# Kernel optimization log

Hardware: AMD Instinct MI355X
Metric: run time of the kernel (lower is better)

## Reference

```python
import jax, jax.numpy as jnp
import numpy as np

B, T, R = 128, 20, 49           # batch, caption length, num regions (7x7)
V, E, H, FD, A = 10000, 512, 512, 512, 256  # vocab, embed, hidden, feature, attn dims


def setup_inputs() -> dict:
    key = jax.random.key(0)
    ks = jax.random.split(key, 16)
    s = 0.02
    return {
        "features": jax.random.normal(ks[0], (B, R, FD), dtype=jnp.float32),
        "captions": jax.random.randint(ks[1], (B, T), 0, V),
        "emb": jax.random.normal(ks[2], (V, E), dtype=jnp.float32) * s,
        "W_h": jax.random.normal(ks[3], (A, H), dtype=jnp.float32) * s,
        "b_h": jnp.zeros((A,), jnp.float32),
        "W_f": jax.random.normal(ks[4], (A, FD), dtype=jnp.float32) * s,
        "b_f": jnp.zeros((A,), jnp.float32),
        "v_w": jax.random.normal(ks[5], (A,), dtype=jnp.float32) * s,
        "v_b": jnp.zeros((), jnp.float32),
        "W_ih": jax.random.normal(ks[6], (4 * H, E + FD), dtype=jnp.float32) * s,
        "W_hh": jax.random.normal(ks[7], (4 * H, H), dtype=jnp.float32) * s,
        "b_ih": jnp.zeros((4 * H,), jnp.float32),
        "b_hh": jnp.zeros((4 * H,), jnp.float32),
        "fc_W": jax.random.normal(ks[8], (V, H), dtype=jnp.float32) * s,
        "fc_b": jnp.zeros((V,), jnp.float32),
    }


def reference(features, captions, emb, W_h, b_h, W_f, b_f, v_w, v_b,
              W_ih, W_hh, b_ih, b_hh, fc_W, fc_b):
    Bn = features.shape[0]
    Hd = W_hh.shape[1]
    # features are constant across timesteps -> project once (same math as per-step W_f(features))
    f_proj = jnp.einsum('brf,af->bra', features, W_f) + b_f  # (B,R,A)
    embeds = emb[captions[:, :-1]]                            # (B,T-1,E)
    xs = jnp.swapaxes(embeds, 0, 1)                           # (T-1,B,E)
    bias = b_ih + b_hh

    def step(carry, x_t):
        hx, cx = carry
        # Bahdanau attention
        h = hx @ W_h.T + b_h                                  # (B,A)
        scores = jnp.tanh(h[:, None, :] + f_proj) @ v_w + v_b  # (B,R)
        alpha = jax.nn.softmax(scores, axis=1)
        context = jnp.einsum('br,brf->bf', alpha, features)   # (B,FD)
        # LSTMCell (PyTorch gate order: i,f,g,o)
        lstm_in = jnp.concatenate([x_t, context], axis=1)     # (B,E+FD)
        gates = lstm_in @ W_ih.T + hx @ W_hh.T + bias         # (B,4H)
        i, f, g, o = jnp.split(gates, 4, axis=1)
        cx = jax.nn.sigmoid(f) * cx + jax.nn.sigmoid(i) * jnp.tanh(g)
        hx = jax.nn.sigmoid(o) * jnp.tanh(cx)
        logit = hx @ fc_W.T + fc_b                            # (B,V)
        return (hx, cx), logit

    init = (jnp.zeros((Bn, Hd), features.dtype), jnp.zeros((Bn, Hd), features.dtype))
    _, logits = jax.lax.scan(step, init, xs)                  # (T-1,B,V)
    return jnp.swapaxes(logits, 0, 1)                         # (B,T-1,V)
```

## Files before the change

### kernel.cpp

```cpp
#include <hip/hip_runtime.h>
#include <hip/hip_bf16.h>
#include <math.h>

#define NB 128
#define NT 20
#define NS 19
#define NR 49
#define NV 10000
#define NE 512
#define NH 512
#define NFD 512
#define NA 256
#define NG 2048
#define NK2 1024

typedef __bf16 bf16_t;
typedef bf16_t bf16x8 __attribute__((ext_vector_type(8)));
typedef bf16_t bf16x4 __attribute__((ext_vector_type(4)));
typedef float f32x4 __attribute__((ext_vector_type(4)));

__device__ __forceinline__ float sigm(float x) { return 1.f / (1.f + expf(-x)); }

__device__ __forceinline__ void cvt8(bf16_t* d, const float* s) {
    float4 a = *(const float4*)s;
    float4 b = *(const float4*)(s + 4);
    bf16x8 v;
    v[0] = (bf16_t)a.x; v[1] = (bf16_t)a.y; v[2] = (bf16_t)a.z; v[3] = (bf16_t)a.w;
    v[4] = (bf16_t)b.x; v[5] = (bf16_t)b.y; v[6] = (bf16_t)b.z; v[7] = (bf16_t)b.w;
    *(bf16x8*)d = v;
}

__global__ __launch_bounds__(256) void k_prep(
    const float* __restrict__ fc_W, const float* __restrict__ W_ih,
    const float* __restrict__ W_hh, const float* __restrict__ W_h,
    const float* __restrict__ W_f, const float* __restrict__ features,
    const float* __restrict__ emb, const int* __restrict__ captions,
    const float* __restrict__ b_ih, const float* __restrict__ b_hh,
    const float* __restrict__ b_f, const float* __restrict__ b_h,
    bf16_t* __restrict__ fcWb, bf16_t* __restrict__ Wcat2,
    bf16_t* __restrict__ Wxg, bf16_t* __restrict__ W_hb,
    bf16_t* __restrict__ Wfb, bf16_t* __restrict__ featb,
    bf16_t* __restrict__ linx, float* __restrict__ bias,
    float* __restrict__ bfh, float* __restrict__ hx, float* __restrict__ cx,
    unsigned* __restrict__ flags)
{
    int g = blockIdx.x * 256 + threadIdx.x;
    if (g < 640000) { int idx = g * 8; cvt8(fcWb + idx, fc_W + idx); return; }
    g -= 640000;
    if (g < 262144) {
        int idx = g * 8;
        int row = idx >> 10, col = idx & 1023;
        int orig = (row & 3) * NH + (row >> 2);
        const float* src = (col < 512) ? (W_ih + (size_t)orig * 1024 + 512 + col)
                                       : (W_hh + (size_t)orig * 512 + (col - 512));
        cvt8(Wcat2 + idx, src);
        return;
    }
    g -= 262144;
    if (g < 131072) {
        int idx = g * 8;
        int row = idx >> 9, col = idx & 511;
        int orig = (row & 3) * NH + (row >> 2);
        cvt8(Wxg + idx, W_ih + (size_t)orig * 1024 + col);
        return;
    }
    g -= 131072;
    if (g < 16384) { int idx = g * 8; cvt8(W_hb + idx, W_h + idx); return; }
    g -= 16384;
    if (g < 16384) { int idx = g * 8; cvt8(Wfb + idx, W_f + idx); return; }
    g -= 16384;
    if (g < 401408) { int idx = g * 8; cvt8(featb + idx, features + idx); return; }
    g -= 401408;
    if (g < 155648) {
        int idx = g * 8;
        int row = idx >> 9, col = idx & 511;
        int t = row >> 7, b = row & 127;
        int cap = captions[b * NT + t];
        cvt8(linx + idx, emb + (size_t)cap * NE + col);
        return;
    }
    g -= 155648;
    if (g < 256) {
        int n0 = g * 8;
        #pragma unroll
        for (int i = 0; i < 8; ++i) {
            int n = n0 + i, h = n >> 2, gg = n & 3;
            int orig = gg * NH + h;
            bias[n] = b_ih[orig] + b_hh[orig];
        }
        return;
    }
    g -= 256;
    if (g < 32) {
        int n0 = g * 8;
        #pragma unroll
        for (int i = 0; i < 8; ++i) bfh[n0 + i] = b_f[n0 + i] + b_h[n0 + i];
        return;
    }
    g -= 32;
    float4 z = make_float4(0.f, 0.f, 0.f, 0.f);
    if (g < 8192) { *(float4*)(hx + g * 8) = z; *(float4*)(hx + g * 8 + 4) = z; return; }
    g -= 8192;
    if (g < 8192) { *(float4*)(cx + g * 8) = z; *(float4*)(cx + g * 8 + 4) = z; return; }
    g -= 8192;
    if (g < 304) {
        #pragma unroll
        for (int i = 0; i < 8; ++i) flags[g * 8 + i] = 0u;
    }
}

__global__ __launch_bounds__(256) void gemm_bf16_nt(
    const bf16_t* __restrict__ Am, const bf16_t* __restrict__ Bm,
    const float* __restrict__ bias, float* __restrict__ Cf,
    bf16_t* __restrict__ Cb, int M, int N, int K, int ldc)
{
    __shared__ uint4 AsU[512];
    __shared__ uint4 BsU[512];
    int tid = threadIdx.x;
    int m0 = blockIdx.x * 64, n0 = blockIdx.y * 64;
    int nk = K >> 6;

    int rowS = tid >> 3, slotS = tid & 7;
    int wr0 = rowS * 8 + (slotS ^ (rowS & 7));
    int rowS2 = rowS + 32;
    int wr1 = rowS2 * 8 + (slotS ^ (rowS2 & 7));

    const uint4* pA = (const uint4*)(Am + (size_t)(m0 + rowS) * K) + slotS;
    size_t aStep = (size_t)4 * K;
    int nrow0 = n0 + rowS, nrow1 = n0 + rowS2;
    bool bv0 = nrow0 < N, bv1 = nrow1 < N;
    const uint4* pB0 = (const uint4*)(Bm + (size_t)nrow0 * K) + slotS;
    const uint4* pB1 = (const uint4*)(Bm + (size_t)nrow1 * K) + slotS;
    uint4 zz = make_uint4(0, 0, 0, 0);

    int w = tid >> 6, lane = tid & 63;
    int wm = w >> 1, wn = w & 1;
    int lr = lane & 15, lg = lane >> 4;
    int ra[2][2], rb[2][2];
    #pragma unroll
    for (int i = 0; i < 2; ++i)
        #pragma unroll
        for (int kk = 0; kk < 2; ++kk) {
            int rA = wm * 32 + i * 16 + lr;
            int rB = wn * 32 + i * 16 + lr;
            int s = kk * 4 + lg;
            ra[i][kk] = rA * 8 + (s ^ (rA & 7));
            rb[i][kk] = rB * 8 + (s ^ (rB & 7));
        }

    f32x4 acc00 = {}, acc01 = {}, acc10 = {}, acc11 = {};
    uint4 a0 = pA[0], a1 = pA[aStep];
    uint4 b0 = bv0 ? pB0[0] : zz;
    uint4 b1 = bv1 ? pB1[0] : zz;
    pA += 8; pB0 += 8; pB1 += 8;

    #pragma unroll 1
    for (int kt = 0; kt < nk; ++kt) {
        __syncthreads();
        AsU[wr0] = a0; AsU[wr1] = a1;
        BsU[wr0] = b0; BsU[wr1] = b1;
        if (kt + 1 < nk) {
            a0 = pA[0]; a1 = pA[aStep];
            b0 = bv0 ? pB0[0] : zz;
            b1 = bv1 ? pB1[0] : zz;
            pA += 8; pB0 += 8; pB1 += 8;
        }
        __syncthreads();
        const bf16x8* Af = (const bf16x8*)AsU;
        const bf16x8* Bf = (const bf16x8*)BsU;
        #pragma unroll
        for (int kk = 0; kk < 2; ++kk) {
            bf16x8 fa0 = Af[ra[0][kk]], fa1 = Af[ra[1][kk]];
            bf16x8 fb0 = Bf[rb[0][kk]], fb1 = Bf[rb[1][kk]];
            acc00 = __builtin_amdgcn_mfma_f32_16x16x32_bf16(fa0, fb0, acc00, 0, 0, 0);
            acc01 = __builtin_amdgcn_mfma_f32_16x16x32_bf16(fa0, fb1, acc01, 0, 0, 0);
            acc10 = __builtin_amdgcn_mfma_f32_16x16x32_bf16(fa1, fb0, acc10, 0, 0, 0);
            acc11 = __builtin_amdgcn_mfma_f32_16x16x32_bf16(fa1, fb1, acc11, 0, 0, 0);
        }
    }

    f32x4 av[2][2] = {{acc00, acc01}, {acc10, acc11}};
    #pragma unroll
    for (int i = 0; i < 2; ++i) {
        int mbase = m0 + wm * 32 + i * 16 + lg * 4;
        #pragma unroll
        for (int j = 0; j < 2; ++j) {
            int n = n0 + wn * 32 + j * 16 + lr;
            if (n < N) {
                float bz = bias ? bias[n] : 0.f;
                #pragma unroll
                for (int r = 0; r < 4; ++r) {
                    float v = av[i][j][r] + bz;
                    if (Cb) Cb[(size_t)(mbase + r) * ldc + n] = (bf16_t)v;
                    else    Cf[(size_t)(mbase + r) * ldc + n] = v;
                }
            }
        }
    }
}

__global__ __launch_bounds__(512) void k_attn(
    const float* __restrict__ hx, const bf16_t* __restrict__ W_hb,
    const bf16_t* __restrict__ fprojb, const float* __restrict__ v_w,
    const bf16_t* __restrict__ featb, bf16_t* __restrict__ lin)
{
    int b = blockIdx.x;
    int tid = threadIdx.x;
    int w = tid >> 6, lane = tid & 63;
    __shared__ float hxs[NH];
    __shared__ float part[2][NA];
    __shared__ float salpha[64];

    hxs[tid] = hx[b * NH + tid];
    __syncthreads();

    {
        int a = tid & 255, q = tid >> 8;
        const bf16x8* wrow = (const bf16x8*)(W_hb + (size_t)a * NH + q * 256);
        const float* hq = hxs + q * 256;
        float p = 0.f;
        #pragma unroll
        for (int c = 0; c < 32; ++c) {
            bf16x8 wv = wrow[c];
            int k = c * 8;
            p += hq[k+0]*(float)wv[0] + hq[k+1]*(float)wv[1]
               + hq[k+2]*(float)wv[2] + hq[k+3]*(float)wv[3]
               + hq[k+4]*(float)wv[4] + hq[k+5]*(float)wv[5]
               + hq[k+6]*(float)wv[6] + hq[k+7]*(float)wv[7];
        }
        part[q][a] = p;
    }
    __syncthreads();

    {
        for (int r = w; r < NR; r += 8) {
            const bf16_t* fp = fprojb + ((size_t)b * NR + r) * NA;
            float s = 0.f;
            #pragma unroll
            for (int j = 0; j < 4; ++j) {
                int aa = lane + 64 * j;
                float hv = part[0][aa] + part[1][aa];
                s += tanhf(hv + (float)fp[aa]) * v_w[aa];
            }
            #pragma unroll
            for (int off = 32; off; off >>= 1) s += __shfl_xor(s, off);
            if (lane == 0) salpha[r] = s;
        }
    }
    __syncthreads();

    if (tid < 64) {
        float v = (tid < NR) ? salpha[tid] : -INFINITY;
        float m = v;
        #pragma unroll
        for (int off = 32; off; off >>= 1) m = fmaxf(m, __shfl_xor(m, off));
        float e = (tid < NR) ? expf(v - m) : 0.f;
        float ssum = e;
        #pragma unroll
        for (int off = 32; off; off >>= 1) ssum += __shfl_xor(ssum, off);
        if (tid < NR) salpha[tid] = e / ssum;
    }
    __syncthreads();

    {
        bf16_t* lrow = lin + (size_t)b * NK2;
        float c = 0.f;
        #pragma unroll 7
        for (int r = 0; r < NR; ++r)
            c += salpha[r] * (float)featb[((size_t)b * NR + r) * NFD + tid];
        lrow[tid] = (bf16_t)c;
        lrow[NFD + tid] = (bf16_t)hxs[tid];
    }
}

__global__ __launch_bounds__(512) void k_fused(
    bf16_t* lin,
    const bf16_t* __restrict__ Wcat2, const bf16_t* __restrict__ pre_x,
    const float* __restrict__ bias, float* hx,
    float* __restrict__ cx, bf16_t* __restrict__ hxAll,
    const bf16_t* __restrict__ W_hb, const bf16_t* __restrict__ fprojb,
    const float* __restrict__ v_w, const bf16_t* __restrict__ featb,
    unsigned* flags, int t, int last)
{
    __shared__ __align__(16) char smem[20736];
    uint4* AsU = (uint4*)smem;
    uint4* BsU = AsU + 256;

    int tid = threadIdx.x;
    int xcd = blockIdx.x & 7, loc = blockIdx.x >> 3;
    int jg = xcd * 4 + (loc & 3);
    int ig = loc >> 2;
    int m0 = ig * 32, n0 = jg * 64;

    int rowS = tid >> 3, slotS = tid & 7;
    int wrB = rowS * 8 + (slotS ^ (rowS & 7));
    bool hasA = rowS < 32;
    int arow = hasA ? (m0 + rowS) : m0;

    const uint4* pB = (const uint4*)(Wcat2 + (size_t)(n0 + rowS) * NK2) + slotS;
    const uint4* pA = (const uint4*)(lin + (size_t)arow * NK2) + slotS;

    int w = tid >> 6, lane = tid & 63;
    int wm = w & 1, wn = w >> 1;
    int lr = lane & 15, lg = lane >> 4;
    int raI[2], rbI[2];
    #pragma unroll
    for (int kk = 0; kk < 2; ++kk) {
        int s = kk * 4 + lg;
        int rA = wm * 16 + lr;
        int rB = wn * 16 + lr;
        raI[kk] = rA * 8 + (s ^ (rA & 7));
        rbI[kk] = rB * 8 + (s ^ (rB & 7));
    }

    f32x4 acc = {};
    uint4 aR = {}, bR = pB[0];
    if (hasA) aR = pA[0];
    pB += 8; pA += 8;

    #pragma unroll 1
    for (int kt = 0; kt < NK2 / 64; ++kt) {
        __syncthreads();
        BsU[wrB] = bR;
        if (hasA) AsU[wrB] = aR;
        if (kt + 1 < NK2 / 64) {
            bR = pB[0]; pB += 8;
            if (hasA) { aR = pA[0]; pA += 8; }
        }
        __syncthreads();
        const bf16x8* Af = (const bf16x8*)AsU;
        const bf16x8* Bf = (const bf16x8*)BsU;
        #pragma unroll
        for (int kk = 0; kk < 2; ++kk) {
            bf16x8 fa = Af[raI[kk]];
            bf16x8 fb = Bf[rbI[kk]];
            acc = __builtin_amdgcn_mfma_f32_16x16x32_bf16(fa, fb, acc, 0, 0, 0);
        }
    }

    __syncthreads();
    float* Ct = (float*)smem;
    {
        int crow = wm * 16 + lg * 4;
        int ccol = wn * 16 + lr;
        #pragma unroll
        for (int r = 0; r < 4; ++r)
            Ct[(crow + r) * 65 + ccol] = acc[r];
    }
    __syncthreads();

    {
        int hloc = tid & 15, m = tid >> 4;
        int bb2 = m0 + m;
        int h = (n0 >> 2) + hloc;
        const float* crow = Ct + m * 65 + hloc * 4;
        const float* brow = bias + n0 + hloc * 4;
        const bf16_t* prow = pre_x + ((size_t)t * NB + bb2) * NG + n0 + hloc * 4;
        float gi = crow[0] + brow[0] + (float)prow[0];
        float gf = crow[1] + brow[1] + (float)prow[1];
        float gg = crow[2] + brow[2] + (float)prow[2];
        float go = crow[3] + brow[3] + (float)prow[3];
        size_t idx = (size_t)bb2 * NH + h;
        float c = sigm(gf) * cx[idx] + sigm(gi) * tanhf(gg);
        float hn = sigm(go) * tanhf(c);
        cx[idx] = c;
        __hip_atomic_store(hx + idx, hn, __ATOMIC_RELAXED,
                           __HIP_MEMORY_SCOPE_AGENT);
        hxAll[((size_t)t * NB + bb2) * NH + h] = (bf16_t)hn;
    }
    if (last) return;

    __syncthreads();
    {
        unsigned* fl = flags + t * 128 + ig * 32;
        if (tid == 0)
            __hip_atomic_store(fl + jg, 1u, __ATOMIC_RELAXED,
                               __HIP_MEMORY_SCOPE_AGENT);
        if (tid < 32) {
            while (__hip_atomic_load(fl + tid, __ATOMIC_RELAXED,
                                     __HIP_MEMORY_SCOPE_AGENT) == 0u)
                __builtin_amdgcn_s_sleep(2);
        }
    }
    __syncthreads();

    int bb = m0 + jg;
    float* hxs  = (float*)smem;
    float* part = hxs + 512;
    float* salp = part + 512;
    float* ctxp = salp + 64;

    hxs[tid] = __hip_atomic_load(hx + (size_t)bb * NH + tid,
                                 __ATOMIC_RELAXED, __HIP_MEMORY_SCOPE_AGENT);
    __syncthreads();

    {
        int a = tid & 255, q = tid >> 8;
        const bf16x8* wrow = (const bf16x8*)(W_hb + (size_t)a * NH + q * 256);
        const float* hq = hxs + q * 256;
        float p = 0.f;
        #pragma unroll
        for (int c = 0; c < 32; ++c) {
            bf16x8 wv = wrow[c];
            int k = c * 8;
            p += hq[k+0]*(float)wv[0] + hq[k+1]*(float)wv[1]
               + hq[k+2]*(float)wv[2] + hq[k+3]*(float)wv[3]
               + hq[k+4]*(float)wv[4] + hq[k+5]*(float)wv[5]
               + hq[k+6]*(float)wv[6] + hq[k+7]*(float)wv[7];
        }
        part[q * 256 + a] = p;
    }
    __syncthreads();
    if (tid < 256) part[tid] += part[256 + tid];
    __syncthreads();

    {
        for (int r = w; r < NR; r += 8) {
            bf16x4 fp4 = *(const bf16x4*)(fprojb + ((size_t)bb * NR + r) * NA + lane * 4);
            float4 vw4 = *(const float4*)(v_w + lane * 4);
            const float* hb = part + lane * 4;
            float s = tanhf(hb[0] + (float)fp4[0]) * vw4.x
                    + tanhf(hb[1] + (float)fp4[1]) * vw4.y
                    + tanhf(hb[2] + (float)fp4[2]) * vw4.z
                    + tanhf(hb[3] + (float)fp4[3]) * vw4.w;
            #pragma unroll
            for (int off = 32; off; off >>= 1) s += __shfl_xor(s, off);
            if (lane == 0) salp[r] = s;
        }
    }
    __syncthreads();

    if (tid < 64) {
        float v = (tid < NR) ? salp[tid] : -INFINITY;
        float m = v;
        #pragma unroll
        for (int off = 32; off; off >>= 1) m = fmaxf(m, __shfl_xor(m, off));
        float e = (tid < NR) ? expf(v - m) : 0.f;
        float ssum = e;
        #pragma unroll
        for (int off = 32; off; off >>= 1) ssum += __shfl_xor(ssum, off);
        if (tid < NR) salp[tid] = e / ssum;
    }
    __syncthreads();

    {
        int ck = tid & 63, rg = tid >> 6;
        float c[8] = {};
        for (int r = rg; r < NR; r += 8) {
            bf16x8 v = *(const bf16x8*)(featb + ((size_t)bb * NR + r) * NFD + ck * 8);
            float al = salp[r];
            #pragma unroll
            for (int jj = 0; jj < 8; ++jj) c[jj] += al * (float)v[jj];
        }
        float* cp = ctxp + (rg * 64 + ck) * 8;
        #pragma unroll
        for (int jj = 0; jj < 8; ++jj) cp[jj] = c[jj];
    }
    __syncthreads();

    {
        float cc = 0.f;
        #pragma unroll
        for (int rg = 0; rg < 8; ++rg) cc += ctxp[rg * 512 + tid];
        bf16_t* lrow = lin + (size_t)bb * NK2;
        lrow[tid]       = (bf16_t)cc;
        lrow[512 + tid] = (bf16_t)hxs[tid];
    }
}

__global__ __launch_bounds__(256) void k_logits(
    const bf16_t* __restrict__ hxAll, const bf16_t* __restrict__ fcWb,
    const float* __restrict__ fc_b, float* __restrict__ out)
{
    const int NWG = 38 * 157, Q = NWG / 8, RR = NWG % 8;
    int bid = blockIdx.x;
    int xcd = bid & 7, loc = bid >> 3;
    int swz = (xcd < RR ? xcd * (Q + 1) : RR * (Q + 1) + (xcd - RR) * Q) + loc;
    int m0 = (swz % 38) * 64;
    int n0 = (swz / 38) * 64;

    __shared__ uint4 AsU[512];
    __shared__ uint4 BsU[512];
    int tid = threadIdx.x;

    int rowS = tid >> 3, slotS = tid & 7;
    int wr0 = rowS * 8 + (slotS ^ (rowS & 7));
    int rowS2 = rowS + 32;
    int wr1 = rowS2 * 8 + (slotS ^ (rowS2 & 7));

    const uint4* pA = (const uint4*)(hxAll + (size_t)(m0 + rowS) * NH) + slotS;
    size_t aStep = (size_t)4 * NH;
    int nrow0 = n0 + rowS, nrow1 = n0 + rowS2;
    bool bv0 = nrow0 < NV, bv1 = nrow1 < NV;
    const uint4* pB0 = (const uint4*)(fcWb + (size_t)nrow0 * NH) + slotS;
    const uint4* pB1 = (const uint4*)(fcWb + (size_t)nrow1 * NH) + slotS;
    uint4 zz = make_uint4(0, 0, 0, 0);

    int w = tid >> 6, lane = tid & 63;
    int wm = w >> 1, wn = w & 1;
    int lr = lane & 15, lg = lane >> 4;
    int ra[2][2], rb[2][2];
    #pragma unroll
    for (int i = 0; i < 2; ++i)
        #pragma unroll
        for (int kk = 0; kk < 2; ++kk) {
            int rA = wm * 32 + i * 16 + lr;
            int rB = wn * 32 + i * 16 + lr;
            int s = kk * 4 + lg;
            ra[i][kk] = rA * 8 + (s ^ (rA & 7));
            rb[i][kk] = rB * 8 + (s ^ (rB & 7));
        }

    f32x4 acc00 = {}, acc01 = {}, acc10 = {}, acc11 = {};
    uint4 a0 = pA[0], a1 = pA[aStep];
    uint4 b0 = bv0 ? pB0[0] : zz;
    uint4 b1 = bv1 ? pB1[0] : zz;
    pA += 8; pB0 += 8; pB1 += 8;

    #pragma unroll 1
    for (int kt = 0; kt < NH / 64; ++kt) {
        __syncthreads();
        AsU[wr0] = a0; AsU[wr1] = a1;
        BsU[wr0] = b0; BsU[wr1] = b1;
        if (kt + 1 < NH / 64) {
            a0 = pA[0]; a1 = pA[aStep];
            b0 = bv0 ? pB0[0] : zz;
            b1 = bv1 ? pB1[0] : zz;
            pA += 8; pB0 += 8; pB1 += 8;
        }
        __syncthreads();
        const bf16x8* Af = (const bf16x8*)AsU;
        const bf16x8* Bf = (const bf16x8*)BsU;
        #pragma unroll
        for (int kk = 0; kk < 2; ++kk) {
            bf16x8 fa0 = Af[ra[0][kk]], fa1 = Af[ra[1][kk]];
            bf16x8 fb0 = Bf[rb[0][kk]], fb1 = Bf[rb[1][kk]];
            acc00 = __builtin_amdgcn_mfma_f32_16x16x32_bf16(fa0, fb0, acc00, 0, 0, 0);
            acc01 = __builtin_amdgcn_mfma_f32_16x16x32_bf16(fa0, fb1, acc01, 0, 0, 0);
            acc10 = __builtin_amdgcn_mfma_f32_16x16x32_bf16(fa1, fb0, acc10, 0, 0, 0);
            acc11 = __builtin_amdgcn_mfma_f32_16x16x32_bf16(fa1, fb1, acc11, 0, 0, 0);
        }
    }

    f32x4 av[2][2] = {{acc00, acc01}, {acc10, acc11}};
    #pragma unroll
    for (int i = 0; i < 2; ++i) {
        int mbase = m0 + wm * 32 + i * 16 + lg * 4;
        #pragma unroll
        for (int j = 0; j < 2; ++j) {
            int n = n0 + wn * 32 + j * 16 + lr;
            if (n < NV) {
                float bz = fc_b[n];
                #pragma unroll
                for (int r = 0; r < 4; ++r) {
                    int m = mbase + r;
                    int bb = m & 127, tt = m >> 7;
                    __builtin_nontemporal_store(
                        av[i][j][r] + bz,
                        out + ((size_t)bb * NS + tt) * NV + n);
                }
            }
        }
    }
}

extern "C" void kernel_launch(void* const* d_in, const int* in_sizes, int n_in,
                              void* d_out, int out_size, void* d_ws, size_t ws_size,
                              hipStream_t stream)
{
    const float* features = (const float*)d_in[0];
    const int*   captions = (const int*)d_in[1];
    const float* emb      = (const float*)d_in[2];
    const float* W_h      = (const float*)d_in[3];
    const float* b_h      = (const float*)d_in[4];
    const float* W_f      = (const float*)d_in[5];
    const float* b_f      = (const float*)d_in[6];
    const float* v_w      = (const float*)d_in[7];
    const float* W_ih     = (const float*)d_in[9];
    const float* W_hh     = (const float*)d_in[10];
    const float* b_ih     = (const float*)d_in[11];
    const float* b_hh     = (const float*)d_in[12];
    const float* fc_W     = (const float*)d_in[13];
    const float* fc_b     = (const float*)d_in[14];
    float* out = (float*)d_out;

    char* base = (char*)d_ws;
    bf16_t* fcWb   = (bf16_t*)base;  base += (size_t)NV * NH * 2;
    bf16_t* Wcat2  = (bf16_t*)base;  base += (size_t)NG * NK2 * 2;
    bf16_t* Wxg    = (bf16_t*)base;  base += (size_t)NG * NE * 2;
    bf16_t* W_hb   = (bf16_t*)base;  base += (size_t)NA * NH * 2;
    bf16_t* Wfb    = (bf16_t*)base;  base += (size_t)NA * NFD * 2;
    bf16_t* featb  = (bf16_t*)base;  base += (size_t)NB * NR * NFD * 2;
    bf16_t* linx   = (bf16_t*)base;  base += (size_t)NS * NB * NE * 2;
    bf16_t* pre_x  = (bf16_t*)base;  base += (size_t)NS * NB * NG * 2;
    bf16_t* lin    = (bf16_t*)base;  base += (size_t)NB * NK2 * 2;
    bf16_t* hxAll  = (bf16_t*)base;  base += (size_t)NS * NB * NH * 2;
    bf16_t* fprojb = (bf16_t*)base;  base += (size_t)NB * NR * NA * 2;
    float*  bias   = (float*)base;   base += (size_t)NG * 4;
    float*  bfh    = (float*)base;   base += (size_t)NA * 4;
    float*  hx     = (float*)base;   base += (size_t)NB * NH * 4;
    float*  cx     = (float*)base;   base += (size_t)NB * NH * 4;
    unsigned* flags = (unsigned*)base; base += (size_t)NS * 128 * 4;

    k_prep<<<dim3(6407), 256, 0, stream>>>(
        fc_W, W_ih, W_hh, W_h, W_f, features, emb, captions, b_ih, b_hh,
        b_f, b_h, fcWb, Wcat2, Wxg, W_hb, Wfb, featb, linx, bias, bfh,
        hx, cx, flags);

    gemm_bf16_nt<<<dim3(98, 4), 256, 0, stream>>>(
        featb, Wfb, bfh, (float*)0, fprojb, NB * NR, NA, NFD, NA);

    gemm_bf16_nt<<<dim3(38, 32), 256, 0, stream>>>(
        linx, Wxg, (const float*)0, (float*)0, pre_x, NS * NB, NG, NE, NG);

    k_attn<<<dim3(NB), 512, 0, stream>>>(hx, W_hb, fprojb, v_w, featb, lin);

    for (int t = 0; t < NS; ++t) {
        k_fused<<<dim3(128), 512, 0, stream>>>(
            lin, Wcat2, pre_x, bias, hx, cx, hxAll,
            W_hb, fprojb, v_w, featb, flags, t, (t == NS - 1) ? 1 : 0);
    }

    k_logits<<<dim3(38 * 157), 256, 0, stream>>>(hxAll, fcWb, fc_b, out);
}
```

Measured before the change: 549.9 us.

## Load gate GEMM K in two large chunks and prefetch features before barrier

```diff
diff --git a/kernel.cpp b/kernel.cpp
--- a/kernel.cpp
+++ b/kernel.cpp
@@ -282,58 +282,71 @@
     const float* __restrict__ v_w, const bf16_t* __restrict__ featb,
     unsigned* flags, int t, int last)
 {
-    __shared__ __align__(16) char smem[20736];
+    __shared__ __align__(16) char smem[98304];
     uint4* AsU = (uint4*)smem;
-    uint4* BsU = AsU + 256;
+    uint4* BsU = AsU + 2048;
 
     int tid = threadIdx.x;
     int xcd = blockIdx.x & 7, loc = blockIdx.x >> 3;
     int jg = xcd * 4 + (loc & 3);
     int ig = loc >> 2;
     int m0 = ig * 32, n0 = jg * 64;
-
-    int rowS = tid >> 3, slotS = tid & 7;
-    int wrB = rowS * 8 + (slotS ^ (rowS & 7));
-    bool hasA = rowS < 32;
-    int arow = hasA ? (m0 + rowS) : m0;
-
-    const uint4* pB = (const uint4*)(Wcat2 + (size_t)(n0 + rowS) * NK2) + slotS;
-    const uint4* pA = (const uint4*)(lin + (size_t)arow * NK2) + slotS;
+    int bb = m0 + jg;
+
+    const uint4* Bg = (const uint4*)(Wcat2 + (size_t)n0 * NK2);
+    const uint4* Ag = (const uint4*)(lin + (size_t)m0 * NK2);
 
     int w = tid >> 6, lane = tid & 63;
     int wm = w & 1, wn = w >> 1;
     int lr = lane & 15, lg = lane >> 4;
-    int raI[2], rbI[2];
-    #pragma unroll
-    for (int kk = 0; kk < 2; ++kk) {
-        int s = kk * 4 + lg;
-        int rA = wm * 16 + lr;
-        int rB = wn * 16 + lr;
-        raI[kk] = rA * 8 + (s ^ (rA & 7));
-        rbI[kk] = rB * 8 + (s ^ (rB & 7));
+
+    uint4 sB[8], sA[4];
+    #pragma unroll
+    for (int c = 0; c < 8; ++c) {
+        int l = tid + 512 * c, row = l >> 6, sl = l & 63;
+        sB[c] = Bg[row * 128 + sl];
+    }
+    #pragma unroll
+    for (int c = 0; c < 4; ++c) {
+        int l = tid + 512 * c, row = l >> 6, sl = l & 63;
+        sA[c] = Ag[row * 128 + sl];
     }
 
     f32x4 acc = {};
-    uint4 aR = {}, bR = pB[0];
-    if (hasA) aR = pA[0];
-    pB += 8; pA += 8;
-
-    #pragma unroll 1
-    for (int kt = 0; kt < NK2 / 64; ++kt) {
+    #pragma unroll
+    for (int it = 0; it < 2; ++it) {
         __syncthreads();
-        BsU[wrB] = bR;
-        if (hasA) AsU[wrB] = aR;
-        if (kt + 1 < NK2 / 64) {
-            bR = pB[0]; pB += 8;
-            if (hasA) { aR = pA[0]; pA += 8; }
+        #pragma unroll
+        for (int c = 0; c < 8; ++c) {
+            int l = tid + 512 * c, row = l >> 6, sl = l & 63;
+            BsU[row * 64 + (sl ^ (row & 7))] = sB[c];
+        }
+        #pragma unroll
+        for (int c = 0; c < 4; ++c) {
+            int l = tid + 512 * c, row = l >> 6, sl = l & 63;
+            AsU[row * 64 + (sl ^ (row & 7))] = sA[c];
         }
         __syncthreads();
+        if (it == 0) {
+            #pragma unroll
+            for (int c = 0; c < 8; ++c) {
+                int l = tid + 512 * c, row = l >> 6, sl = l & 63;
+                sB[c] = Bg[row * 128 + 64 + sl];
+            }
+            #pragma unroll
+            for (int c = 0; c < 4; ++c) {
+                int l = tid + 512 * c, row = l >> 6, sl = l & 63;
+                sA[c] = Ag[row * 128 + 64 + sl];
+            }
+        }
         const bf16x8* Af = (const bf16x8*)AsU;
         const bf16x8* Bf = (const bf16x8*)BsU;
-        #pragma unroll
-        for (int kk = 0; kk < 2; ++kk) {
-            bf16x8 fa = Af[raI[kk]];
-            bf16x8 fb = Bf[rbI[kk]];
+        int rA = wm * 16 + lr, rB = wn * 16 + lr;
+        #pragma unroll
+        for (int kk = 0; kk < 16; ++kk) {
+            int s = kk * 4 + lg;
+            bf16x8 fa = Af[rA * 64 + (s ^ (rA & 7))];
+            bf16x8 fb = Bf[rB * 64 + (s ^ (rB & 7))];
             acc = __builtin_amdgcn_mfma_f32_16x16x32_bf16(fa, fb, acc, 0, 0, 0);
         }
     }
@@ -370,6 +383,19 @@
     }
     if (last) return;
 
+    int ck = tid & 63, rg = tid >> 6;
+    bf16x8 fbr[7];
+    #pragma unroll
+    for (int k = 0; k < 7; ++k) {
+        int r = rg + 8 * k;
+        if (r < NR)
+            fbr[k] = *(const bf16x8*)(featb + ((size_t)bb * NR + r) * NFD + ck * 8);
+        else {
+            bf16x8 zv = {};
+            fbr[k] = zv;
+        }
+    }
+
     __syncthreads();
     {
         unsigned* fl = flags + t * 128 + ig * 32;
@@ -384,7 +410,6 @@
     }
     __syncthreads();
 
-    int bb = m0 + jg;
     float* hxs  = (float*)smem;
     float* part = hxs + 512;
     float* salp = part + 512;
@@ -444,13 +469,15 @@
     __syncthreads();
 
     {
-        int ck = tid & 63, rg = tid >> 6;
         float c[8] = {};
-        for (int r = rg; r < NR; r += 8) {
-            bf16x8 v = *(const bf16x8*)(featb + ((size_t)bb * NR + r) * NFD + ck * 8);
-            float al = salp[r];
-            #pragma unroll
-            for (int jj = 0; jj < 8; ++jj) c[jj] += al * (float)v[jj];
+        #pragma unroll
+        for (int k = 0; k < 7; ++k) {
+            int r = rg + 8 * k;
+            if (r < NR) {
+                float al = salp[r];
+                #pragma unroll
+                for (int jj = 0; jj < 8; ++jj) c[jj] += al * (float)fbr[k][jj];
+            }
         }
         float* cp = ctxp + (rg * 64 + ck) * 8;
         #pragma unroll
@@ -461,7 +488,7 @@
     {
         float cc = 0.f;
         #pragma unroll
-        for (int rg = 0; rg < 8; ++rg) cc += ctxp[rg * 512 + tid];
+        for (int rg2 = 0; rg2 < 8; ++rg2) cc += ctxp[rg2 * 512 + tid];
         bf16_t* lrow = lin + (size_t)bb * NK2;
         lrow[tid]       = (bf16_t)cc;
         lrow[512 + tid] = (bf16_t)hxs[tid];
```

Result: slower. 910.8 us (+65.6%).
